# Kernel optimization log

Measured on AMD Instinct MI355X. Metric: run time of the kernel, lower is better.

## Reference

```python
import jax, jax.numpy as jnp
import numpy as np
import math

V, E, H, A, N = 32000, 512, 512, 64, 8  # vocab, embed, rnn hidden, att_size, n_heads
T, B = 256, 128                          # scan length (acts as att batch), inner dim


def _lstm(x, Wih, Whh, bih, bhh):
    # x: (T, B, E); torch nn.LSTM gate order i, f, g, o; zero initial state
    Bb = x.shape[1]
    Hh = Whh.shape[1]
    init = (jnp.zeros((Bb, Hh), x.dtype), jnp.zeros((Bb, Hh), x.dtype))

    def step(carry, xt):
        h, c = carry
        gates = xt @ Wih.T + bih + h @ Whh.T + bhh          # (B, 4H)
        i, f, g, o = jnp.split(gates, 4, axis=-1)
        c = jax.nn.sigmoid(f) * c + jax.nn.sigmoid(i) * jnp.tanh(g)
        h = jax.nn.sigmoid(o) * jnp.tanh(c)
        return (h, c), h

    _, hs = jax.lax.scan(step, init, x)
    return hs  # (T, B, H)


def setup_inputs() -> dict:
    key = jax.random.key(0)
    ks = jax.random.split(key, 26)
    rn = lambda k, s: jax.random.normal(k, s, jnp.float32) * 0.02
    inp = {
        "input_seq_l": jax.random.randint(ks[0], (T, B), 0, V, jnp.int32),
        "input_seq_r": jax.random.randint(ks[1], (T, B), 0, V, jnp.int32),
        "emb_l": rn(ks[2], (V, E)),
        "emb_r": rn(ks[3], (V, E)),
        "Wih_l": rn(ks[4], (4 * H, E)), "Whh_l": rn(ks[5], (4 * H, H)),
        "bih_l": rn(ks[6], (4 * H,)), "bhh_l": rn(ks[7], (4 * H,)),
        "Wih_r": rn(ks[8], (4 * H, E)), "Whh_r": rn(ks[9], (4 * H, H)),
        "bih_r": rn(ks[10], (4 * H,)), "bhh_r": rn(ks[11], (4 * H,)),
        "Wq": rn(ks[12], (N, H, A)), "bq": rn(ks[13], (N, A)),
        "Wk": rn(ks[14], (N, H, A)), "bk": rn(ks[15], (N, A)),
        "Wv": rn(ks[16], (N, H, A)), "bv": rn(ks[17], (N, A)),
        "Wo": rn(ks[18], (N * A, H)), "bo": rn(ks[19], (H,)),
        "Wh": rn(ks[20], (2 * H, 64)), "bh": rn(ks[21], (64,)),
        "Wa": rn(ks[22], (64, 2)), "ba": rn(ks[23], (2,)),
    }
    return inp


def reference(input_seq_l, input_seq_r, emb_l, emb_r,
              Wih_l, Whh_l, bih_l, bhh_l,
              Wih_r, Whh_r, bih_r, bhh_r,
              Wq, bq, Wk, bk, Wv, bv, Wo, bo, Wh, bh, Wa, ba):
    # left encoder
    ol = _lstm(emb_l[input_seq_l], Wih_l, Whh_l, bih_l, bhh_l)   # (T, B, H)
    # multi-head attention over left outputs (all heads batched)
    q = jnp.einsum('tbh,nhd->ntbd', ol, Wq) + bq[:, None, None, :]
    k = jnp.einsum('tbh,nhd->ntbd', ol, Wk) + bk[:, None, None, :]
    v = jnp.einsum('tbh,nhd->ntbd', ol, Wv) + bv[:, None, None, :]
    scores = jnp.einsum('ntbd,ntcd->ntbc', q, k) / math.sqrt(A)  # (N, T, B, B)
    p = jax.nn.softmax(scores, axis=-1)
    att = jnp.einsum('ntbc,ntcd->ntbd', p, v)                    # (N, T, B, A)
    att = att.transpose(1, 2, 0, 3).reshape(att.shape[1], att.shape[2], -1)  # (T, B, N*A)
    ol = att @ Wo + bo                                           # (T, B, H)
    ol = ol.mean(axis=1)                                         # (T, H)
    # right encoder
    orr = _lstm(emb_r[input_seq_r], Wih_r, Whh_r, bih_r, bhh_r).mean(axis=1)  # (T, H)
    cat = jnp.concatenate([ol, orr], axis=1)                     # (T, 2H)
    fc = cat @ Wh + bh
    ans = jax.nn.softmax(fc @ Wa + ba, axis=1)                   # (T, 2)
    return ans
```

## Files before the change

kernel.cpp:

```cpp
#include <hip/hip_runtime.h>

typedef unsigned short u16;
typedef __attribute__((ext_vector_type(4))) float f32x4;
typedef __attribute__((ext_vector_type(8))) short bf8;

#define MFMA16(a, b, c) __builtin_amdgcn_mfma_f32_16x16x32_bf16((a), (b), (c), 0, 0, 0)

__device__ __forceinline__ u16 f2bf(float f) {
  unsigned u = __builtin_bit_cast(unsigned, f);
  u += 0x7FFFu + ((u >> 16) & 1u);
  return (u16)(u >> 16);
}
__device__ __forceinline__ float bf2f(u16 h) {
  unsigned u = ((unsigned)h) << 16;
  return __builtin_bit_cast(float, u);
}
__device__ __forceinline__ float sigm(float x) { return 1.0f / (1.0f + __expf(-x)); }
__device__ __forceinline__ float tanh_f(float x) {
  x = fminf(fmaxf(x, -15.f), 15.f);
  float e = __expf(2.f * x);
  return (e - 1.f) / (e + 1.f);
}

__global__ void k_fill(float* __restrict__ p, int n, float v) {
  int i = blockIdx.x * blockDim.x + threadIdx.x;
  if (i < n) p[i] = v;
}

__device__ __forceinline__ void gemm_body(
    const int* __restrict__ idx, const float* __restrict__ emb,
    const float* __restrict__ Wih, u16* __restrict__ Gpre,
    int m_base, int m0, int n0, char* smem, int tid) {
  u16 (*lA)[72] = (u16(*)[72])smem;
  u16 (*lB)[72] = (u16(*)[72])(smem + 18432);
  int lane = tid & 63, wid = tid >> 6;
  int wm = (wid >> 1) << 6, wn = (wid & 1) << 6;
  int lq = lane >> 4, lc = lane & 15;
  f32x4 acc[4][4] = {};
  for (int k0 = 0; k0 < 512; k0 += 64) {
#pragma unroll
    for (int s = 0; s < 2; s++) {
      int slot = tid + s * 256;
      int row = slot >> 2, seg = (slot & 3) << 4;
      const float* pa = emb + (size_t)idx[m_base + m0 + row] * 512 + k0 + seg;
      const float* pb = Wih + (size_t)(n0 + row) * 512 + k0 + seg;
      float4 a0 = ((const float4*)pa)[0], a1 = ((const float4*)pa)[1];
      float4 a2 = ((const float4*)pa)[2], a3 = ((const float4*)pa)[3];
      float4 b0 = ((const float4*)pb)[0], b1 = ((const float4*)pb)[1];
      float4 b2 = ((const float4*)pb)[2], b3 = ((const float4*)pb)[3];
      union { u16 h[8]; int4 v; } pk;
      pk.h[0]=f2bf(a0.x); pk.h[1]=f2bf(a0.y); pk.h[2]=f2bf(a0.z); pk.h[3]=f2bf(a0.w);
      pk.h[4]=f2bf(a1.x); pk.h[5]=f2bf(a1.y); pk.h[6]=f2bf(a1.z); pk.h[7]=f2bf(a1.w);
      *(int4*)&lA[row][seg] = pk.v;
      pk.h[0]=f2bf(a2.x); pk.h[1]=f2bf(a2.y); pk.h[2]=f2bf(a2.z); pk.h[3]=f2bf(a2.w);
      pk.h[4]=f2bf(a3.x); pk.h[5]=f2bf(a3.y); pk.h[6]=f2bf(a3.z); pk.h[7]=f2bf(a3.w);
      *(int4*)&lA[row][seg + 8] = pk.v;
      pk.h[0]=f2bf(b0.x); pk.h[1]=f2bf(b0.y); pk.h[2]=f2bf(b0.z); pk.h[3]=f2bf(b0.w);
      pk.h[4]=f2bf(b1.x); pk.h[5]=f2bf(b1.y); pk.h[6]=f2bf(b1.z); pk.h[7]=f2bf(b1.w);
      *(int4*)&lB[row][seg] = pk.v;
      pk.h[0]=f2bf(b2.x); pk.h[1]=f2bf(b2.y); pk.h[2]=f2bf(b2.z); pk.h[3]=f2bf(b2.w);
      pk.h[4]=f2bf(b3.x); pk.h[5]=f2bf(b3.y); pk.h[6]=f2bf(b3.z); pk.h[7]=f2bf(b3.w);
      *(int4*)&lB[row][seg + 8] = pk.v;
    }
    __syncthreads();
#pragma unroll
    for (int kk = 0; kk < 64; kk += 32) {
      int ko = kk + (lq << 3);
      bf8 af[4], bg[4];
#pragma unroll
      for (int i = 0; i < 4; i++) af[i] = *(const bf8*)&lA[wm + i * 16 + lc][ko];
#pragma unroll
      for (int j = 0; j < 4; j++) bg[j] = *(const bf8*)&lB[wn + j * 16 + lc][ko];
#pragma unroll
      for (int i = 0; i < 4; i++)
#pragma unroll
        for (int j = 0; j < 4; j++) acc[i][j] = MFMA16(af[i], bg[j], acc[i][j]);
    }
    __syncthreads();
  }
  int cr = lq << 2;
#pragma unroll
  for (int i = 0; i < 4; i++)
#pragma unroll
    for (int j = 0; j < 4; j++)
#pragma unroll
      for (int r = 0; r < 4; r++) {
        int m = m0 + wm + i * 16 + cr + r;
        int nn = n0 + wn + j * 16 + lc;
        Gpre[(size_t)m * 2048 + nn] = f2bf(acc[i][j][r]);
      }
}

__global__ __launch_bounds__(256, 2) void k_prep(
    unsigned* __restrict__ flg, float* __restrict__ hrm,
    const float* __restrict__ Whh_l, u16* __restrict__ Whl,
    const float* __restrict__ Whh_r, u16* __restrict__ Whr,
    const float* __restrict__ bih_l, const float* __restrict__ bhh_l, float* __restrict__ bsl,
    const float* __restrict__ bih_r, const float* __restrict__ bhh_r, float* __restrict__ bsr,
    const int* __restrict__ seq_l, const int* __restrict__ seq_r,
    const float* __restrict__ emb_l, const float* __restrict__ emb_r,
    const float* __restrict__ Wih_l, const float* __restrict__ Wih_r,
    u16* __restrict__ Gl0, u16* __restrict__ Gr0, int Tc0) {
  __shared__ __align__(16) char smem[36864];
  int bid = blockIdx.x, tid = threadIdx.x;
  if (bid < 2) {
    flg[bid * 256 + tid] = 0u;
  } else if (bid < 514) {
    hrm[(bid - 2) * 256 + tid] = 0.f;
  } else if (bid < 2562) {
    int rel = bid - 514;
    int enc = rel >> 10;
    int i = (rel & 1023) * 256 + tid;
    const float* in = enc ? Whh_r : Whh_l;
    u16* outp = enc ? Whr : Whl;
    float4 v = ((const float4*)in)[i];
    union { u16 h[4]; uint2 u; } p;
    p.h[0] = f2bf(v.x); p.h[1] = f2bf(v.y); p.h[2] = f2bf(v.z); p.h[3] = f2bf(v.w);
    ((uint2*)outp)[i] = p.u;
  } else if (bid < 2578) {
    int rel = bid - 2562;
    int enc = rel >> 3;
    int i = (rel & 7) * 256 + tid;
    if (enc == 0) bsl[i] = bih_l[i] + bhh_l[i];
    else          bsr[i] = bih_r[i] + bhh_r[i];
  } else {
    int rel = bid - 2578;
    int per = Tc0 << 4;
    int ge = rel >= per;
    int rem = ge ? rel - per : rel;
    gemm_body(ge ? seq_r : seq_l, ge ? emb_r : emb_l, ge ? Wih_r : Wih_l,
              ge ? Gr0 : Gl0, 0, (rem >> 4) << 7, (rem & 15) << 7, smem, tid);
  }
}

__device__ void lstm_body(
    const u16* __restrict__ Gl, const u16* __restrict__ Gr,
    const u16* __restrict__ Whl, const u16* __restrict__ Whr,
    const float* __restrict__ bsl, const float* __restrict__ bsr,
    u16* __restrict__ hsl, float* __restrict__ hrm,
    unsigned* __restrict__ hx, float* __restrict__ cstate,
    unsigned* __restrict__ flg, int t0, int nT, char* hlds, int bid, int tid) {
  int pod = bid & 7, cg = bid >> 3;
  int e = pod >> 2, bg = pod & 3;
  int b0 = bg << 5, c0 = cg << 5;
  const u16* Gpre = e ? Gr : Gl;
  const u16* Whh  = e ? Whr : Whl;
  const float* bsum = e ? bsr : bsl;

  int lane = tid & 63, w = tid >> 6;
  int lq = lane >> 4, lc = lane & 15, cr = lq << 2;
  int cl = (w << 3) + (lc & 7);
  int gg0 = lc >> 3;
  int lr0 = (gg0 << 5) + cl;
  int lr1 = ((2 + gg0) << 5) + cl;
  int gc0 = (gg0 << 9) + c0 + cl;
  int gc1 = ((2 + gg0) << 9) + c0 + cl;
  float bs0 = bsum[gc0], bs1 = bsum[gc1];
  bool owner = (lc & 8) != 0;

  int gr0 = ((lr0 >> 5) << 9) + c0 + (lr0 & 31);
  int gr1 = ((lr1 >> 5) << 9) + c0 + (lr1 & 31);
  bf8 wb0[16], wb1[16];
  {
    const u16* p0 = Whh + (size_t)gr0 * 512 + (lq << 3);
    const u16* p1 = Whh + (size_t)gr1 * 512 + (lq << 3);
#pragma unroll
    for (int ks = 0; ks < 16; ks++) {
      wb0[ks] = *(const bf8*)(p0 + (ks << 5));
      wb1[ks] = *(const bf8*)(p1 + (ks << 5));
    }
  }
  float creg[2][4];
#pragma unroll
  for (int mi = 0; mi < 2; mi++)
#pragma unroll
    for (int r = 0; r < 4; r++) creg[mi][r] = 0.f;
  if (t0 > 0 && owner) {
#pragma unroll
    for (int mi = 0; mi < 2; mi++)
#pragma unroll
      for (int r = 0; r < 4; r++)
        creg[mi][r] = cstate[(size_t)((e << 7) + b0 + (mi << 4) + cr + r) * 512 + c0 + cl];
  }

  u16 gp[2][2][4];
#pragma unroll
  for (int mi = 0; mi < 2; mi++)
#pragma unroll
    for (int r = 0; r < 4; r++) {
      size_t rowb = (size_t)(b0 + (mi << 4) + cr + r) << 11;
      gp[mi][0][r] = Gpre[rowb + gc0];
      gp[mi][1][r] = Gpre[rowb + gc1];
    }

  int ax = (lc & 7) << 4;
  int abyte0 = lc << 10;
  int abyte1 = (16 + lc) << 10;
  int hxc = (c0 >> 1) + (w << 2) + ((lc & 7) >> 1);
  const int srow = tid >> 6;
  const int scolb = (tid & 63) << 4;

  for (int t = 0; t < nT; t++) {
    int tg = t0 + t;
    f32x4 acc[2][2] = {};
    if (tg > 0) {
      if (t > 0) {
        if (tid < 64) {
          const unsigned* fa = flg + (pod << 6) + (lane & 15);
          unsigned fv;
          int guard = 0;
          while (true) {
            asm volatile("global_load_dword %0, %1, off sc0 sc1"
                         : "=v"(fv) : "v"(fa) : "memory");
            asm volatile("s_waitcnt vmcnt(0)" ::: "memory");
            if (__ballot(fv >= (unsigned)tg) == ~0ull) break;
            if (++guard > 300000) break;
          }
        }
        __syncthreads();
      }
      const unsigned* hxr = hx + (((size_t)((e << 1) | ((tg - 1) & 1))) << 15);
      uint4 sv[8];
#pragma unroll
      for (int i = 0; i < 8; i++) {
        int row = (i << 2) + srow;
        const unsigned* ap = hxr + (((size_t)(b0 + row)) << 8) + ((tid & 63) << 2);
        asm volatile("global_load_dwordx4 %0, %1, off sc0 sc1"
                     : "=v"(sv[i]) : "v"(ap));
      }
      asm volatile("s_waitcnt vmcnt(0)" ::: "memory");
      __builtin_amdgcn_sched_barrier(0);
#pragma unroll
      for (int i = 0; i < 8; i++) {
        int row = (i << 2) + srow;
        *(uint4*)(hlds + (row << 10) + (scolb ^ ((row & 7) << 4))) = sv[i];
      }
      __syncthreads();
#pragma unroll
      for (int ks = 0; ks < 16; ks++) {
        int kb = (ks << 6) + (lq << 4);
        bf8 a0 = *(const bf8*)(hlds + abyte0 + (kb ^ ax));
        bf8 a1 = *(const bf8*)(hlds + abyte1 + (kb ^ ax));
        acc[0][0] = MFMA16(a0, wb0[ks], acc[0][0]);
        acc[0][1] = MFMA16(a0, wb1[ks], acc[0][1]);
        acc[1][0] = MFMA16(a1, wb0[ks], acc[1][0]);
        acc[1][1] = MFMA16(a1, wb1[ks], acc[1][1]);
      }
      __syncthreads();
    }
    unsigned* hxw = hx + (((size_t)((e << 1) | (tg & 1))) << 15);
    float msum = 0.f;
#pragma unroll
    for (int mi = 0; mi < 2; mi++)
#pragma unroll
      for (int r = 0; r < 4; r++) {
        float v0 = acc[mi][0][r] + bf2f(gp[mi][0][r]) + bs0;
        float v1 = acc[mi][1][r] + bf2f(gp[mi][1][r]) + bs1;
        float send = sigm(v0) * tanh_f(v1);
        float recv = __shfl_xor(send, 8, 64);
        float h = 0.f;
        if (owner) {
          float c = sigm(v0) * creg[mi][r] + recv;
          creg[mi][r] = c;
          h = sigm(v1) * tanh_f(c);
          msum += h;
        }
        unsigned hb = (unsigned)f2bf(h);
        unsigned hi = __shfl_down(hb, 1, 64);
        unsigned packed = (hb & 0xffffu) | (hi << 16);
        int b = b0 + (mi << 4) + cr + r;
        if (owner && !(lane & 1)) {
          if (!e)
            *(unsigned*)(hsl + (((size_t)((tg << 7) + b)) << 9) + c0 + cl) = packed;
          unsigned* sa = hxw + (((size_t)b) << 8) + hxc;
          asm volatile("global_store_dword %0, %1, off sc0 sc1"
                       :: "v"(sa), "v"(packed) : "memory");
        }
      }
    asm volatile("s_waitcnt vmcnt(0)" ::: "memory");
    __syncthreads();
    if (tid == 0) {
      unsigned tv = (unsigned)(tg + 1);
      unsigned* fa = flg + (pod << 6) + cg;
      asm volatile("global_store_dword %0, %1, off sc0 sc1"
                   :: "v"(fa), "v"(tv) : "memory");
    }
    if (e) {
      float s = msum;
      s += __shfl_xor(s, 16, 64);
      s += __shfl_xor(s, 32, 64);
      if (owner && lq == 0)
        atomicAdd(&hrm[(tg << 9) + c0 + cl], s * 0.0078125f);
    }
    if (t + 1 < nT) {
#pragma unroll
      for (int mi = 0; mi < 2; mi++)
#pragma unroll
        for (int r = 0; r < 4; r++) {
          size_t rowb = (size_t)(((t + 1) << 7) + b0 + (mi << 4) + cr + r) << 11;
          gp[mi][0][r] = Gpre[rowb + gc0];
          gp[mi][1][r] = Gpre[rowb + gc1];
        }
    }
  }
  if (owner) {
#pragma unroll
    for (int mi = 0; mi < 2; mi++)
#pragma unroll
      for (int r = 0; r < 4; r++)
        cstate[(size_t)((e << 7) + b0 + (mi << 4) + cr + r) * 512 + c0 + cl] = creg[mi][r];
  }
}

__global__ __launch_bounds__(256, 1) void k_fused(
    const u16* __restrict__ Gl, const u16* __restrict__ Gr,
    u16* __restrict__ Ggl, u16* __restrict__ Ggr,
    const int* __restrict__ seq_l, const int* __restrict__ seq_r,
    const float* __restrict__ emb_l, const float* __restrict__ emb_r,
    const float* __restrict__ Wih_l, const float* __restrict__ Wih_r,
    const u16* __restrict__ Whl, const u16* __restrict__ Whr,
    const float* __restrict__ bsl, const float* __restrict__ bsr,
    u16* __restrict__ hsl, float* __restrict__ hrm,
    unsigned* __restrict__ hx, float* __restrict__ cstate,
    unsigned* __restrict__ flg,
    const float* __restrict__ Wq, const float* __restrict__ Wk, const float* __restrict__ Wv,
    u16* __restrict__ WqT, u16* __restrict__ WkT, u16* __restrict__ WvT,
    int t0, int nT, int gmb, int nextT) {
  __shared__ __align__(16) char smem[81920];
  int bid = blockIdx.x, tid = threadIdx.x;
  if (bid < 128) {
    lstm_body(Gl, Gr, Whl, Whr, bsl, bsr, hsl, hrm, hx, cstate, flg,
              t0, nT, smem, bid, tid);
  } else {
    int gb = bid - 128;
    int per2 = nextT << 5;
    if (gb < per2) {
      int per = nextT << 4;
      int ge = gb >= per;
      int rem = ge ? gb - per : gb;
      gemm_body(ge ? seq_r : seq_l, ge ? emb_r : emb_l, ge ? Wih_r : Wih_l,
                ge ? Ggr : Ggl, gmb, (rem >> 4) << 7, (rem & 15) << 7, smem, tid);
    } else {
      int rel = gb - per2;
      int which = rel >> 10;
      int g = (rel & 1023) * 256 + tid;
      const float* W = which == 0 ? Wq : (which == 1 ? Wk : Wv);
      u16* WT = which == 0 ? WqT : (which == 1 ? WkT : WvT);
      int n = g >> 15, d = (g >> 9) & 63, h = g & 511;
      WT[g] = f2bf(W[(n << 15) + (h << 6) + d]);
    }
  }
}

__global__ __launch_bounds__(256, 1) void k_attn(
    const u16* __restrict__ hs,
    const u16* __restrict__ WqT, const u16* __restrict__ WkT, const u16* __restrict__ WvT,
    const float* __restrict__ bq, const float* __restrict__ bk, const float* __restrict__ bv,
    float* __restrict__ attmean) {
  __shared__ __align__(16) char smem[123904];
  u16 (*qs)[72]  = (u16(*)[72])smem;
  u16 (*ksm)[72] = (u16(*)[72])(smem + 18432);
  u16 (*vt)[136] = (u16(*)[136])(smem + 36864);
  float (*sc)[132] = (float(*)[132])(smem + 54272);
  u16 (*ps)[136] = (u16(*)[136])smem;
  float* red = (float*)(smem + 54272);
  float* pmax = (float*)(smem + 121856);
  float* psum = (float*)(smem + 122880);

  int bid = blockIdx.x;
  int n = bid >> 8, t = bid & 255;
  int tid = threadIdx.x, lane = tid & 63, wid = tid >> 6;
  int lq = lane >> 4, lc = lane & 15, cr = lq << 2;
  const u16* ol = hs + ((size_t)t << 16);

  float bqv[4], bkv[4];
#pragma unroll
  for (int nf = 0; nf < 4; nf++) {
    bqv[nf] = bq[(n << 6) + (nf << 4) + lc];
    bkv[nf] = bk[(n << 6) + (nf << 4) + lc];
  }
  float bvv[4][4];
#pragma unroll
  for (int mi = 0; mi < 4; mi++)
#pragma unroll
    for (int r = 0; r < 4; r++) bvv[mi][r] = bv[(n << 6) + (mi << 4) + cr + r];

  const u16* wq = WqT + ((size_t)n << 15);
  const u16* wk = WkT + ((size_t)n << 15);
  const u16* wv = WvT + ((size_t)n << 15);
  f32x4 aq[2][4] = {}, ak[2][4] = {}, av[4][2] = {};
  for (int ks = 0; ks < 16; ks++) {
    int ko = (ks << 5) + (lq << 3);
    bf8 a0 = *(const bf8*)&ol[(size_t)((wid << 5) + lc) * 512 + ko];
    bf8 a1 = *(const bf8*)&ol[(size_t)((wid << 5) + 16 + lc) * 512 + ko];
#pragma unroll
    for (int nf = 0; nf < 4; nf++) {
      bf8 bw = *(const bf8*)&wq[(size_t)((nf << 4) + lc) * 512 + ko];
      aq[0][nf] = MFMA16(a0, bw, aq[0][nf]);
      aq[1][nf] = MFMA16(a1, bw, aq[1][nf]);
      bf8 bw2 = *(const bf8*)&wk[(size_t)((nf << 4) + lc) * 512 + ko];
      ak[0][nf] = MFMA16(a0, bw2, ak[0][nf]);
      ak[1][nf] = MFMA16(a1, bw2, ak[1][nf]);
    }
#pragma unroll
    for (int mi = 0; mi < 4; mi++) {
      bf8 aw = *(const bf8*)&wv[(size_t)((mi << 4) + lc) * 512 + ko];
      av[mi][0] = MFMA16(aw, a0, av[mi][0]);
      av[mi][1] = MFMA16(aw, a1, av[mi][1]);
    }
  }
#pragma unroll
  for (int mi = 0; mi < 2; mi++)
#pragma unroll
    for (int nf = 0; nf < 4; nf++)
#pragma unroll
      for (int r = 0; r < 4; r++) {
        int b = (wid << 5) + (mi << 4) + cr + r;
        int d = (nf << 4) + lc;
        qs[b][d] = f2bf(aq[mi][nf][r] + bqv[nf]);
        ksm[b][d] = f2bf(ak[mi][nf][r] + bkv[nf]);
      }
#pragma unroll
  for (int mi = 0; mi < 4; mi++)
#pragma unroll
    for (int c2 = 0; c2 < 2; c2++)
#pragma unroll
      for (int r = 0; r < 4; r++) {
        int d = (mi << 4) + cr + r;
        int c = (wid << 5) + (c2 << 4) + lc;
        vt[d][c] = f2bf(av[mi][c2][r] + bvv[mi][r]);
      }
  __syncthreads();

  f32x4 as_[2][8] = {};
#pragma unroll
  for (int ks = 0; ks < 2; ks++) {
    int ko = (ks << 5) + (lq << 3);
    bf8 a0 = *(const bf8*)&qs[(wid << 5) + lc][ko];
    bf8 a1 = *(const bf8*)&qs[(wid << 5) + 16 + lc][ko];
#pragma unroll
    for (int nf = 0; nf < 8; nf++) {
      bf8 bw = *(const bf8*)&ksm[(nf << 4) + lc][ko];
      as_[0][nf] = MFMA16(a0, bw, as_[0][nf]);
      as_[1][nf] = MFMA16(a1, bw, as_[1][nf]);
    }
  }
#pragma unroll
  for (int mi = 0; mi < 2; mi++)
#pragma unroll
    for (int nf = 0; nf < 8; nf++)
#pragma unroll
      for (int r = 0; r < 4; r++)
        sc[(wid << 5) + (mi << 4) + cr + r][(nf << 4) + lc] = as_[mi][nf][r] * 0.125f;
  __syncthreads();

  {
    int row = tid & 127, half = tid >> 7;
    int cb = half << 6;
    float mx = -1e30f;
    for (int j = 0; j < 64; j++) mx = fmaxf(mx, sc[row][cb + j]);
    pmax[(half << 7) + row] = mx;
    __syncthreads();
    mx = fmaxf(pmax[row], pmax[128 + row]);
    float s = 0.f;
    for (int j = 0; j < 64; j++) { float ev = __expf(sc[row][cb + j] - mx); s += ev; sc[row][cb + j] = ev; }
    psum[(half << 7) + row] = s;
    __syncthreads();
    float inv = 1.f / (psum[row] + psum[128 + row]);
    for (int j = 0; j < 64; j++) ps[row][cb + j] = f2bf(sc[row][cb + j] * inv);
  }
  __syncthreads();

  f32x4 ao[2][4] = {};
#pragma unroll
  for (int ks = 0; ks < 4; ks++) {
    int ko = (ks << 5) + (lq << 3);
    bf8 a0 = *(const bf8*)&ps[(wid << 5) + lc][ko];
    bf8 a1 = *(const bf8*)&ps[(wid << 5) + 16 + lc][ko];
#pragma unroll
    for (int nf = 0; nf < 4; nf++) {
      bf8 bw = *(const bf8*)&vt[(nf << 4) + lc][ko];
      ao[0][nf] = MFMA16(a0, bw, ao[0][nf]);
      ao[1][nf] = MFMA16(a1, bw, ao[1][nf]);
    }
  }
  float pm[4];
#pragma unroll
  for (int nf = 0; nf < 4; nf++) {
    float s = 0.f;
#pragma unroll
    for (int mi = 0; mi < 2; mi++)
#pragma unroll
      for (int r = 0; r < 4; r++) s += ao[mi][nf][r];
    s += __shfl_xor(s, 16, 64);
    s += __shfl_xor(s, 32, 64);
    pm[nf] = s;
  }
  if (lq == 0) {
#pragma unroll
    for (int nf = 0; nf < 4; nf++) red[(wid << 6) + (nf << 4) + lc] = pm[nf];
  }
  __syncthreads();
  if (tid < 64) {
    float s = red[tid] + red[64 + tid] + red[128 + tid] + red[192 + tid];
    attmean[(t << 9) + (n << 6) + tid] = s * 0.0078125f;
  }
}

__global__ __launch_bounds__(256) void k_olm(const float* __restrict__ am, const float* __restrict__ Wo,
                                             const float* __restrict__ bo, float* __restrict__ olm) {
  __shared__ float row[512];
  int t = blockIdx.x >> 1, h0 = (blockIdx.x & 1) << 8;
  int tid = threadIdx.x;
  row[tid] = am[(t << 9) + tid];
  row[tid + 256] = am[(t << 9) + 256 + tid];
  __syncthreads();
  int h = h0 + tid;
  float s = bo[h];
  for (int k = 0; k < 512; k++) s += row[k] * Wo[(k << 9) + h];
  olm[(t << 9) + h] = s;
}

__global__ __launch_bounds__(64) void k_final(const float* __restrict__ olmp, const float* __restrict__ hrm,
                                              const float* __restrict__ Wh, const float* __restrict__ bh,
                                              const float* __restrict__ Wa, const float* __restrict__ ba,
                                              float* __restrict__ out) {
  __shared__ float cat[1024];
  int t = blockIdx.x, j = threadIdx.x;
  for (int i = j; i < 512; i += 64) {
    cat[i] = olmp[(t << 9) + i];
    cat[512 + i] = hrm[(t << 9) + i];
  }
  __syncthreads();
  float f = bh[j];
  for (int k = 0; k < 1024; k++) f += cat[k] * Wh[(k << 6) + j];
  float p0 = f * Wa[j * 2], p1 = f * Wa[j * 2 + 1];
#pragma unroll
  for (int o = 32; o > 0; o >>= 1) { p0 += __shfl_down(p0, o); p1 += __shfl_down(p1, o); }
  if (j == 0) {
    p0 += ba[0]; p1 += ba[1];
    float m = fmaxf(p0, p1);
    float e0 = __expf(p0 - m), e1 = __expf(p1 - m);
    float inv = 1.f / (e0 + e1);
    out[t * 2] = e0 * inv;
    out[t * 2 + 1] = e1 * inv;
  }
}

extern "C" void kernel_launch(void* const* d_in, const int* in_sizes, int n_in,
                              void* d_out, int out_size, void* d_ws, size_t ws_size,
                              hipStream_t stream) {
  const int*   seq_l = (const int*)d_in[0];
  const int*   seq_r = (const int*)d_in[1];
  const float* emb_l = (const float*)d_in[2];
  const float* emb_r = (const float*)d_in[3];
  const float* Wih_l = (const float*)d_in[4];
  const float* Whh_l = (const float*)d_in[5];
  const float* bih_l = (const float*)d_in[6];
  const float* bhh_l = (const float*)d_in[7];
  const float* Wih_r = (const float*)d_in[8];
  const float* Whh_r = (const float*)d_in[9];
  const float* bih_r = (const float*)d_in[10];
  const float* bhh_r = (const float*)d_in[11];
  const float* Wq = (const float*)d_in[12];
  const float* bq = (const float*)d_in[13];
  const float* Wk = (const float*)d_in[14];
  const float* bk = (const float*)d_in[15];
  const float* Wv = (const float*)d_in[16];
  const float* bv = (const float*)d_in[17];
  const float* Wo = (const float*)d_in[18];
  const float* bo = (const float*)d_in[19];
  const float* Wh = (const float*)d_in[20];
  const float* bhc = (const float*)d_in[21];
  const float* Wa = (const float*)d_in[22];
  const float* ba = (const float*)d_in[23];
  float* out = (float*)d_out;

  char* ws = (char*)d_ws;
  size_t off = 0;
  auto alloc = [&](size_t bytes) { char* p = ws + off; off += (bytes + 255) & ~(size_t)255; return p; };
  u16*   hsl  = (u16*)alloc(33554432);
  u16*   Whl  = (u16*)alloc(2097152);
  u16*   Whr  = (u16*)alloc(2097152);
  u16*   WqT  = (u16*)alloc(524288);
  u16*   WkT  = (u16*)alloc(524288);
  u16*   WvT  = (u16*)alloc(524288);
  float* bsl  = (float*)alloc(8192);
  float* bsr  = (float*)alloc(8192);
  unsigned* hx = (unsigned*)alloc(524288);
  float* cst  = (float*)alloc(524288);
  unsigned* flg = (unsigned*)alloc(2048);
  float* am   = (float*)alloc(524288);
  float* hrm  = (float*)alloc(524288);
  float* olm  = (float*)alloc(524288);
  size_t fixed = off;

  int chunks[4]; int nch = 0; int Tmax = 0;
  if (fixed + 4ull * 128 * 524288ull <= ws_size) {
    chunks[0] = 128; chunks[1] = 128; nch = 2; Tmax = 128;
  } else if (fixed + 4ull * 96 * 524288ull <= ws_size) {
    chunks[0] = 96; chunks[1] = 96; chunks[2] = 64; nch = 3; Tmax = 96;
  } else if (fixed + 4ull * 64 * 524288ull <= ws_size) {
    chunks[0] = chunks[1] = chunks[2] = chunks[3] = 64; nch = 4; Tmax = 64;
  } else {
    k_fill<<<2, 256, 0, stream>>>(out, out_size, 0.25f);
    return;
  }
  size_t gbytes = (size_t)Tmax * 524288ull;
  u16* Glb[2]; u16* Grb[2];
  Glb[0] = (u16*)alloc(gbytes); Glb[1] = (u16*)alloc(gbytes);
  Grb[0] = (u16*)alloc(gbytes); Grb[1] = (u16*)alloc(gbytes);

  k_prep<<<2578 + (chunks[0] << 5), 256, 0, stream>>>(
      flg, hrm, Whh_l, Whl, Whh_r, Whr,
      bih_l, bhh_l, bsl, bih_r, bhh_r, bsr,
      seq_l, seq_r, emb_l, emb_r, Wih_l, Wih_r, Glb[0], Grb[0], chunks[0]);

  int t0 = 0;
  for (int c = 0; c < nch; c++) {
    int nT = chunks[c];
    int nextT = (c + 1 < nch) ? chunks[c + 1] : 0;
    int grid = 128 + (nextT << 5) + (c == 0 ? 3072 : 0);
    k_fused<<<grid, 256, 0, stream>>>(
        Glb[c & 1], Grb[c & 1], Glb[(c + 1) & 1], Grb[(c + 1) & 1],
        seq_l, seq_r, emb_l, emb_r, Wih_l, Wih_r,
        Whl, Whr, bsl, bsr, hsl, hrm, hx, cst, flg,
        Wq, Wk, Wv, WqT, WkT, WvT,
        t0, nT, (t0 + nT) << 7, nextT);
    t0 += nT;
  }
  k_attn<<<2048, 256, 0, stream>>>(hsl, WqT, WkT, WvT, bq, bk, bv, am);
  k_olm<<<512, 256, 0, stream>>>(am, Wo, bo, olm);
  k_final<<<256, 64, 0, stream>>>(olm, hrm, Wh, bhc, Wa, ba, out);
}
```

Measured before the change: 1.761 ms.

## Overlap attention for finished chunks with the next LSTM chunk

Attention blocks for the previous chunk's timesteps now run inside the fused LSTM kernel alongside the recurrence, and only the last chunk's attention runs in a separate kernel afterwards. The Wq/Wk/Wv bf16 transpose moves into the prep kernel. The LSTM flag wait now has every wave poll its own source flags instead of one wave polling followed by a block barrier, and the h loads are remapped so each wave reads the columns it waits on. This is meant to hide attention work behind the latency-bound recurrence. In exchange the fused kernel's shared memory grows to about 124KB, and co-resident attention blocks may compete with the 128 recurrence blocks for CUs and memory bandwidth.

Result: slower. 1.880 ms (+6.8%).

```diff
diff --git a/kernel.cpp b/kernel.cpp
--- a/kernel.cpp
+++ b/kernel.cpp
@@ -95,6 +95,9 @@
     unsigned* __restrict__ flg, float* __restrict__ hrm,
     const float* __restrict__ Whh_l, u16* __restrict__ Whl,
     const float* __restrict__ Whh_r, u16* __restrict__ Whr,
+    const float* __restrict__ Wq, u16* __restrict__ WqT,
+    const float* __restrict__ Wk, u16* __restrict__ WkT,
+    const float* __restrict__ Wv, u16* __restrict__ WvT,
     const float* __restrict__ bih_l, const float* __restrict__ bhh_l, float* __restrict__ bsl,
     const float* __restrict__ bih_r, const float* __restrict__ bhh_r, float* __restrict__ bsr,
     const int* __restrict__ seq_l, const int* __restrict__ seq_r,
@@ -117,14 +120,22 @@
     union { u16 h[4]; uint2 u; } p;
     p.h[0] = f2bf(v.x); p.h[1] = f2bf(v.y); p.h[2] = f2bf(v.z); p.h[3] = f2bf(v.w);
     ((uint2*)outp)[i] = p.u;
-  } else if (bid < 2578) {
+  } else if (bid < 5634) {
     int rel = bid - 2562;
+    int which = rel >> 10;
+    int g = (rel & 1023) * 256 + tid;
+    const float* W = which == 0 ? Wq : (which == 1 ? Wk : Wv);
+    u16* WT = which == 0 ? WqT : (which == 1 ? WkT : WvT);
+    int n = g >> 15, d = (g >> 9) & 63, h = g & 511;
+    WT[g] = f2bf(W[(n << 15) + (h << 6) + d]);
+  } else if (bid < 5650) {
+    int rel = bid - 5634;
     int enc = rel >> 3;
     int i = (rel & 7) * 256 + tid;
     if (enc == 0) bsl[i] = bih_l[i] + bhh_l[i];
     else          bsr[i] = bih_r[i] + bhh_r[i];
   } else {
-    int rel = bid - 2578;
+    int rel = bid - 5650;
     int per = Tc0 << 4;
     int ge = rel >= per;
     int rem = ge ? rel - per : rel;
@@ -197,34 +208,33 @@
   int abyte0 = lc << 10;
   int abyte1 = (16 + lc) << 10;
   int hxc = (c0 >> 1) + (w << 2) + ((lc & 7) >> 1);
-  const int srow = tid >> 6;
-  const int scolb = (tid & 63) << 4;
+  const int c4 = (w << 4) + (lane >> 2);
+  const int rsub = lane & 3;
+  const int scolb = c4 << 4;
+  const int srcm = (w << 2) + (lane >> 4);
 
   for (int t = 0; t < nT; t++) {
     int tg = t0 + t;
     f32x4 acc[2][2] = {};
     if (tg > 0) {
-      if (t > 0) {
-        if (tid < 64) {
-          const unsigned* fa = flg + (pod << 6) + (lane & 15);
-          unsigned fv;
-          int guard = 0;
-          while (true) {
-            asm volatile("global_load_dword %0, %1, off sc0 sc1"
-                         : "=v"(fv) : "v"(fa) : "memory");
-            asm volatile("s_waitcnt vmcnt(0)" ::: "memory");
-            if (__ballot(fv >= (unsigned)tg) == ~0ull) break;
-            if (++guard > 300000) break;
-          }
+      {
+        const unsigned* fa = flg + (pod << 6) + srcm;
+        unsigned fv;
+        int guard = 0;
+        while (true) {
+          asm volatile("global_load_dword %0, %1, off sc0 sc1"
+                       : "=v"(fv) : "v"(fa) : "memory");
+          asm volatile("s_waitcnt vmcnt(0)" ::: "memory");
+          if (__ballot(fv >= (unsigned)tg) == ~0ull) break;
+          if (++guard > 300000) break;
         }
-        __syncthreads();
       }
       const unsigned* hxr = hx + (((size_t)((e << 1) | ((tg - 1) & 1))) << 15);
       uint4 sv[8];
 #pragma unroll
       for (int i = 0; i < 8; i++) {
-        int row = (i << 2) + srow;
-        const unsigned* ap = hxr + (((size_t)(b0 + row)) << 8) + ((tid & 63) << 2);
+        int row = (i << 2) + rsub;
+        const unsigned* ap = hxr + (((size_t)(b0 + row)) << 8) + (c4 << 2);
         asm volatile("global_load_dwordx4 %0, %1, off sc0 sc1"
                      : "=v"(sv[i]) : "v"(ap));
       }
@@ -232,7 +242,7 @@
       __builtin_amdgcn_sched_barrier(0);
 #pragma unroll
       for (int i = 0; i < 8; i++) {
-        int row = (i << 2) + srow;
+        int row = (i << 2) + rsub;
         *(uint4*)(hlds + (row << 10) + (scolb ^ ((row & 7) << 4))) = sv[i];
       }
       __syncthreads();
@@ -312,52 +322,11 @@
   }
 }
 
-__global__ __launch_bounds__(256, 1) void k_fused(
-    const u16* __restrict__ Gl, const u16* __restrict__ Gr,
-    u16* __restrict__ Ggl, u16* __restrict__ Ggr,
-    const int* __restrict__ seq_l, const int* __restrict__ seq_r,
-    const float* __restrict__ emb_l, const float* __restrict__ emb_r,
-    const float* __restrict__ Wih_l, const float* __restrict__ Wih_r,
-    const u16* __restrict__ Whl, const u16* __restrict__ Whr,
-    const float* __restrict__ bsl, const float* __restrict__ bsr,
-    u16* __restrict__ hsl, float* __restrict__ hrm,
-    unsigned* __restrict__ hx, float* __restrict__ cstate,
-    unsigned* __restrict__ flg,
-    const float* __restrict__ Wq, const float* __restrict__ Wk, const float* __restrict__ Wv,
-    u16* __restrict__ WqT, u16* __restrict__ WkT, u16* __restrict__ WvT,
-    int t0, int nT, int gmb, int nextT) {
-  __shared__ __align__(16) char smem[81920];
-  int bid = blockIdx.x, tid = threadIdx.x;
-  if (bid < 128) {
-    lstm_body(Gl, Gr, Whl, Whr, bsl, bsr, hsl, hrm, hx, cstate, flg,
-              t0, nT, smem, bid, tid);
-  } else {
-    int gb = bid - 128;
-    int per2 = nextT << 5;
-    if (gb < per2) {
-      int per = nextT << 4;
-      int ge = gb >= per;
-      int rem = ge ? gb - per : gb;
-      gemm_body(ge ? seq_r : seq_l, ge ? emb_r : emb_l, ge ? Wih_r : Wih_l,
-                ge ? Ggr : Ggl, gmb, (rem >> 4) << 7, (rem & 15) << 7, smem, tid);
-    } else {
-      int rel = gb - per2;
-      int which = rel >> 10;
-      int g = (rel & 1023) * 256 + tid;
-      const float* W = which == 0 ? Wq : (which == 1 ? Wk : Wv);
-      u16* WT = which == 0 ? WqT : (which == 1 ? WkT : WvT);
-      int n = g >> 15, d = (g >> 9) & 63, h = g & 511;
-      WT[g] = f2bf(W[(n << 15) + (h << 6) + d]);
-    }
-  }
-}
-
-__global__ __launch_bounds__(256, 1) void k_attn(
+__device__ void attn_body(
     const u16* __restrict__ hs,
     const u16* __restrict__ WqT, const u16* __restrict__ WkT, const u16* __restrict__ WvT,
     const float* __restrict__ bq, const float* __restrict__ bk, const float* __restrict__ bv,
-    float* __restrict__ attmean) {
-  __shared__ __align__(16) char smem[123904];
+    float* __restrict__ attmean, int n, int t, char* smem, int tid) {
   u16 (*qs)[72]  = (u16(*)[72])smem;
   u16 (*ksm)[72] = (u16(*)[72])(smem + 18432);
   u16 (*vt)[136] = (u16(*)[136])(smem + 36864);
@@ -367,9 +336,7 @@
   float* pmax = (float*)(smem + 121856);
   float* psum = (float*)(smem + 122880);
 
-  int bid = blockIdx.x;
-  int n = bid >> 8, t = bid & 255;
-  int tid = threadIdx.x, lane = tid & 63, wid = tid >> 6;
+  int lane = tid & 63, wid = tid >> 6;
   int lq = lane >> 4, lc = lane & 15, cr = lq << 2;
   const u16* ol = hs + ((size_t)t << 16);
 
@@ -505,6 +472,54 @@
     float s = red[tid] + red[64 + tid] + red[128 + tid] + red[192 + tid];
     attmean[(t << 9) + (n << 6) + tid] = s * 0.0078125f;
   }
+}
+
+__global__ __launch_bounds__(256, 1) void k_fused(
+    const u16* __restrict__ Gl, const u16* __restrict__ Gr,
+    u16* __restrict__ Ggl, u16* __restrict__ Ggr,
+    const int* __restrict__ seq_l, const int* __restrict__ seq_r,
+    const float* __restrict__ emb_l, const float* __restrict__ emb_r,
+    const float* __restrict__ Wih_l, const float* __restrict__ Wih_r,
+    const u16* __restrict__ Whl, const u16* __restrict__ Whr,
+    const float* __restrict__ bsl, const float* __restrict__ bsr,
+    u16* __restrict__ hsl, float* __restrict__ hrm,
+    unsigned* __restrict__ hx, float* __restrict__ cstate,
+    unsigned* __restrict__ flg,
+    const u16* __restrict__ WqT, const u16* __restrict__ WkT, const u16* __restrict__ WvT,
+    const float* __restrict__ bq, const float* __restrict__ bk, const float* __restrict__ bv,
+    float* __restrict__ am,
+    int t0, int nT, int gmb, int nextT, int prev_t0) {
+  __shared__ __align__(16) char smem[123904];
+  int bid = blockIdx.x, tid = threadIdx.x;
+  if (bid < 128) {
+    lstm_body(Gl, Gr, Whl, Whr, bsl, bsr, hsl, hrm, hx, cstate, flg,
+              t0, nT, smem, bid, tid);
+  } else {
+    int gb = bid - 128;
+    int gemmN = nextT << 5;
+    if (gb < gemmN) {
+      int per = nextT << 4;
+      int ge = gb >= per;
+      int rem = ge ? gb - per : gb;
+      gemm_body(ge ? seq_r : seq_l, ge ? emb_r : emb_l, ge ? Wih_r : Wih_l,
+                ge ? Ggr : Ggl, gmb, (rem >> 4) << 7, (rem & 15) << 7, smem, tid);
+    } else {
+      int ab = gb - gemmN;
+      attn_body(hsl, WqT, WkT, WvT, bq, bk, bv, am, ab & 7, prev_t0 + (ab >> 3),
+                smem, tid);
+    }
+  }
+}
+
+__global__ __launch_bounds__(256, 1) void k_attn(
+    const u16* __restrict__ hs,
+    const u16* __restrict__ WqT, const u16* __restrict__ WkT, const u16* __restrict__ WvT,
+    const float* __restrict__ bq, const float* __restrict__ bk, const float* __restrict__ bv,
+    float* __restrict__ attmean, int t0) {
+  __shared__ __align__(16) char smem[123904];
+  int bid = blockIdx.x;
+  attn_body(hs, WqT, WkT, WvT, bq, bk, bv, attmean, bid & 7, t0 + (bid >> 3),
+            smem, threadIdx.x);
 }
 
 __global__ __launch_bounds__(256) void k_olm(const float* __restrict__ am, const float* __restrict__ Wo,
@@ -611,8 +626,8 @@
   Glb[0] = (u16*)alloc(gbytes); Glb[1] = (u16*)alloc(gbytes);
   Grb[0] = (u16*)alloc(gbytes); Grb[1] = (u16*)alloc(gbytes);
 
-  k_prep<<<2578 + (chunks[0] << 5), 256, 0, stream>>>(
-      flg, hrm, Whh_l, Whl, Whh_r, Whr,
+  k_prep<<<5650 + (chunks[0] << 5), 256, 0, stream>>>(
+      flg, hrm, Whh_l, Whl, Whh_r, Whr, Wq, WqT, Wk, WkT, Wv, WvT,
       bih_l, bhh_l, bsl, bih_r, bhh_r, bsr,
       seq_l, seq_r, emb_l, emb_r, Wih_l, Wih_r, Glb[0], Grb[0], chunks[0]);
 
@@ -620,16 +635,19 @@
   for (int c = 0; c < nch; c++) {
     int nT = chunks[c];
     int nextT = (c + 1 < nch) ? chunks[c + 1] : 0;
-    int grid = 128 + (nextT << 5) + (c == 0 ? 3072 : 0);
+    int prevT = (c > 0) ? chunks[c - 1] : 0;
+    int grid = 128 + (nextT << 5) + (prevT << 3);
     k_fused<<<grid, 256, 0, stream>>>(
         Glb[c & 1], Grb[c & 1], Glb[(c + 1) & 1], Grb[(c + 1) & 1],
         seq_l, seq_r, emb_l, emb_r, Wih_l, Wih_r,
         Whl, Whr, bsl, bsr, hsl, hrm, hx, cst, flg,
-        Wq, Wk, Wv, WqT, WkT, WvT,
-        t0, nT, (t0 + nT) << 7, nextT);
+        WqT, WkT, WvT, bq, bk, bv, am,
+        t0, nT, (t0 + nT) << 7, nextT, t0 - prevT);
     t0 += nT;
   }
-  k_attn<<<2048, 256, 0, stream>>>(hsl, WqT, WkT, WvT, bq, bk, bv, am);
+  int lastT = chunks[nch - 1];
+  k_attn<<<lastT << 3, 256, 0, stream>>>(hsl, WqT, WkT, WvT, bq, bk, bv, am,
+                                         256 - lastT);
   k_olm<<<512, 256, 0, stream>>>(am, Wo, bo, olm);
   k_final<<<256, 64, 0, stream>>>(olm, hrm, Wh, bhc, Wa, ba, out);
 }
```
